# Kernel optimization log

Hardware: AMD Instinct MI355X
Metric: run time of the kernel (lower is better)

The kernel has to match this reference:

```python
import jax, jax.numpy as jnp
import numpy as np

NSTEPS = 64  # Euler integration steps for the CPAB ODE solve


def cpab_basis_1d(nC):
    """Null-space basis of the continuity constraints for a 1D CPAB
    tessellation with nC cells (velocity a_c*x + b_c per cell, continuous
    at interior knots, no zero-boundary constraint). Returns [2*nC, nC+1]."""
    d = 2 * nC
    L = np.zeros((nC - 1, d), dtype=np.float64)
    for k in range(1, nC):  # small fixed loop over cells
        xk = k / nC
        L[k - 1, 2 * (k - 1):2 * k] = [xk, 1.0]
        L[k - 1, 2 * k:2 * k + 2] = [-xk, -1.0]
    _, _, Vt = np.linalg.svd(L)
    return np.ascontiguousarray(Vt[nC - 1:].T).astype(np.float32)  # [2nC, nC+1]


def setup_inputs() -> dict:
    key = jax.random.key(0)
    k1, k2 = jax.random.split(key)
    B, Lin, C, nC = 256, 2048, 32, 32
    x = jax.random.normal(k1, (B, Lin, C), dtype=jnp.float32)
    theta = 0.5 * jax.random.normal(k2, (B, nC + 1), dtype=jnp.float32)
    basis = jnp.asarray(cpab_basis_1d(nC))  # [64, 33]
    return {"x": x, "theta": theta, "basis": basis, "out_len": 2048}


def reference(x, theta, basis, out_len):
    # x: [B, Lin, C]; theta: [B, d]; basis: [2*nC, d]
    B, Lin, C = x.shape
    nC = basis.shape[0] // 2
    dt = 1.0 / NSTEPS

    # Per-cell affine velocity coefficients: v_c(x) = a_c * x + b_c
    A = jnp.einsum('kd,bd->bk', basis, theta).reshape(B, nC, 2)
    Aa, Ab = A[..., 0], A[..., 1]  # each [B, nC]

    # Integrate dphi/dt = v(phi) from the uniform grid on [0,1]
    grid = jnp.linspace(0.0, 1.0, out_len, dtype=x.dtype)
    phi0 = jnp.broadcast_to(grid, (B, out_len))

    def step(phi, _):
        idx = jnp.clip(jnp.floor(phi * nC).astype(jnp.int32), 0, nC - 1)
        a = jnp.take_along_axis(Aa, idx, axis=1)
        b = jnp.take_along_axis(Ab, idx, axis=1)
        return phi + (a * phi + b) * dt, None

    phi, _ = jax.lax.scan(step, phi0, None, length=NSTEPS)

    # Linear resampling of x at the warped grid
    p = jnp.clip(phi, 0.0, 1.0) * (Lin - 1)           # [B, out_len]
    i0 = jnp.clip(jnp.floor(p).astype(jnp.int32), 0, Lin - 2)
    w = (p - i0.astype(p.dtype))[..., None]           # [B, out_len, 1]
    g0 = jnp.take_along_axis(x, i0[..., None], axis=1)        # [B, out_len, C]
    g1 = jnp.take_along_axis(x, (i0 + 1)[..., None], axis=1)  # [B, out_len, C]
    return g0 * (1.0 - w) + g1 * w
```

## Files before the change

kernel.cpp:

```cpp
#include <hip/hip_runtime.h>


#define NSTEPS 64
#define NC     32
#define DD     33
#define LIN    2048
#define CCH    32
#define OUTLEN 2048
#define JPW    64
#define WPB    4
#define JPB    (JPW * WPB)

typedef float f32x4 __attribute__((ext_vector_type(4)));

__global__ __launch_bounds__(256) void cpab_warp_kernel(
    const float* __restrict__ x,
    const float* __restrict__ theta,
    const float* __restrict__ basis,
    float* __restrict__ out)
{
    __shared__ float2 ctab[WPB][NC];
    __shared__ float2 iw[WPB][JPW];

    const int t    = threadIdx.x;
    const int wave = t >> 6;
    const int lane = t & 63;
    const int blocksPerB = OUTLEN / JPB;
    const int b     = blockIdx.x / blocksPerB;
    const int jbase = (blockIdx.x % blocksPerB) * JPB + wave * JPW;

    const float dt = 1.0f / (float)NSTEPS;

    float acc = 0.0f;
    {
        const float* bs = basis + lane * DD;
        const float* th = theta + b * DD;
        #pragma unroll
        for (int d = 0; d < DD; ++d) acc = fmaf(bs[d], th[d], acc);
    }
    {
        int c = lane & (NC - 1);
        float a  = __shfl(acc, 2 * c);
        float bb = __shfl(acc, 2 * c + 1);
        if (lane < NC) ctab[wave][c] = make_float2(fmaf(a, dt, 1.0f), bb * dt * (float)NC);
    }

    {
        const int j = jbase + lane;
        float q = (float)j * ((float)NC / (float)(OUTLEN - 1));
        const float2* ct = ctab[wave];
        #pragma unroll
        for (int s = 0; s < NSTEPS; ++s) {
            float f = fminf(fmaxf(q, 0.0f), (float)(NC - 1));
            float2 cc = ct[(int)f];
            q = fmaf(cc.x, q, cc.y);
        }
        float p = fminf(fmaxf(q * ((float)(LIN - 1) / (float)NC), 0.0f), (float)(LIN - 1));
        int i0 = min((int)p, LIN - 2);
        iw[wave][lane] = make_float2(p - (float)i0, (float)i0);
    }

    const f32x4* xb = (const f32x4*)(x + (size_t)b * (LIN * CCH));
    f32x4* ob = (f32x4*)(out + ((size_t)b * OUTLEN + jbase) * CCH);
    const int c4  = lane & 7;
    const int jl0 = lane >> 3;

    float2 f[8];
    #pragma unroll
    for (int it = 0; it < 8; ++it) f[it] = iw[wave][it * 8 + jl0];

    f32x4 g0[8], g1[8];
    #pragma unroll
    for (int it = 0; it < 8; ++it) {
        int i0 = (int)f[it].y;
        g0[it] = xb[i0 * (CCH / 4) + c4];
        g1[it] = xb[(i0 + 1) * (CCH / 4) + c4];
    }
    __builtin_amdgcn_sched_barrier(0);

    #pragma unroll
    for (int it = 0; it < 8; ++it) {
        float w = f[it].x;
        f32x4 r = g0[it] + w * (g1[it] - g0[it]);
        __builtin_nontemporal_store(r, &ob[(it * 8 + jl0) * (CCH / 4) + c4]);
    }
}

extern "C" void kernel_launch(void* const* d_in, const int* in_sizes, int n_in,
                              void* d_out, int out_size, void* d_ws, size_t ws_size,
                              hipStream_t stream) {
    const float* x     = (const float*)d_in[0];
    const float* theta = (const float*)d_in[1];
    const float* basis = (const float*)d_in[2];
    float* out = (float*)d_out;

    const int B = in_sizes[1] / DD;
    const int grid = B * (OUTLEN / JPB);
    cpab_warp_kernel<<<grid, 256, 0, stream>>>(x, theta, basis, out);
}
```

Before: 28.34 us.

## Halve outputs per wave and remap blocks so each batch stays on one XCD

Each wave now handles 32 output positions instead of 64, which doubles the grid to 4096 blocks and gives more parallelism and latency hiding. Block indices are remapped so that all 16 blocks of a batch element land on the same XCD (assuming round-robin dispatch over 8 XCDs), which should improve L2 reuse of that batch's input rows. The cost is that half the lanes run the 64-step ODE loop redundantly, and the per-wave coefficient-table setup is repeated across twice as many waves. The mapping hardcodes B as a multiple of 8 and 16 blocks per batch.

```diff
diff --git a/kernel.cpp b/kernel.cpp
--- a/kernel.cpp
+++ b/kernel.cpp
@@ -7,9 +7,11 @@
 #define LIN    2048
 #define CCH    32
 #define OUTLEN 2048
-#define JPW    64
+#define JPW    32
 #define WPB    4
 #define JPB    (JPW * WPB)
+#define BPB    (OUTLEN / JPB)
+#define NXCD   8
 
 typedef float f32x4 __attribute__((ext_vector_type(4)));
 
@@ -25,9 +27,14 @@
     const int t    = threadIdx.x;
     const int wave = t >> 6;
     const int lane = t & 63;
-    const int blocksPerB = OUTLEN / JPB;
-    const int b     = blockIdx.x / blocksPerB;
-    const int jbase = (blockIdx.x % blocksPerB) * JPB + wave * JPW;
+
+    const int d    = blockIdx.x;
+    const int xcd  = d & (NXCD - 1);
+    const int r    = d >> 3;
+    const int part = r & (BPB - 1);
+    const int bh   = r >> 4;
+    const int b     = bh * NXCD + xcd;
+    const int jbase = part * JPB + wave * JPW;
 
     const float dt = 1.0f / (float)NSTEPS;
 
@@ -36,7 +43,7 @@
         const float* bs = basis + lane * DD;
         const float* th = theta + b * DD;
         #pragma unroll
-        for (int d = 0; d < DD; ++d) acc = fmaf(bs[d], th[d], acc);
+        for (int dd = 0; dd < DD; ++dd) acc = fmaf(bs[dd], th[dd], acc);
     }
     {
         int c = lane & (NC - 1);
@@ -46,7 +53,8 @@
     }
 
     {
-        const int j = jbase + lane;
+        const int jl = lane & (JPW - 1);
+        const int j  = jbase + jl;
         float q = (float)j * ((float)NC / (float)(OUTLEN - 1));
         const float2* ct = ctab[wave];
         #pragma unroll
@@ -57,7 +65,7 @@
         }
         float p = fminf(fmaxf(q * ((float)(LIN - 1) / (float)NC), 0.0f), (float)(LIN - 1));
         int i0 = min((int)p, LIN - 2);
-        iw[wave][lane] = make_float2(p - (float)i0, (float)i0);
+        if (lane < JPW) iw[wave][jl] = make_float2(p - (float)i0, (float)i0);
     }
 
     const f32x4* xb = (const f32x4*)(x + (size_t)b * (LIN * CCH));
@@ -65,13 +73,13 @@
     const int c4  = lane & 7;
     const int jl0 = lane >> 3;
 
-    float2 f[8];
+    float2 f[JPW / 8];
     #pragma unroll
-    for (int it = 0; it < 8; ++it) f[it] = iw[wave][it * 8 + jl0];
+    for (int it = 0; it < JPW / 8; ++it) f[it] = iw[wave][it * 8 + jl0];
 
-    f32x4 g0[8], g1[8];
+    f32x4 g0[JPW / 8], g1[JPW / 8];
     #pragma unroll
-    for (int it = 0; it < 8; ++it) {
+    for (int it = 0; it < JPW / 8; ++it) {
         int i0 = (int)f[it].y;
         g0[it] = xb[i0 * (CCH / 4) + c4];
         g1[it] = xb[(i0 + 1) * (CCH / 4) + c4];
@@ -79,10 +87,10 @@
     __builtin_amdgcn_sched_barrier(0);
 
     #pragma unroll
-    for (int it = 0; it < 8; ++it) {
+    for (int it = 0; it < JPW / 8; ++it) {
         float w = f[it].x;
-        f32x4 r = g0[it] + w * (g1[it] - g0[it]);
-        __builtin_nontemporal_store(r, &ob[(it * 8 + jl0) * (CCH / 4) + c4]);
+        f32x4 rr = g0[it] + w * (g1[it] - g0[it]);
+        __builtin_nontemporal_store(rr, &ob[(it * 8 + jl0) * (CCH / 4) + c4]);
     }
 }
 
@@ -95,6 +103,6 @@
     float* out = (float*)d_out;
 
     const int B = in_sizes[1] / DD;
-    const int grid = B * (OUTLEN / JPB);
+    const int grid = B * BPB;
     cpab_warp_kernel<<<grid, 256, 0, stream>>>(x, theta, basis, out);
 }
```

Result: slower. 32.60 us (+15.1%).
